# Optimization experiments

Measured on AMD Instinct MI355X. Metric: run time of the kernel, lower is better.

The kernel has to match this reference:

```python
import jax, jax.numpy as jnp
import numpy as np

B, N, K, DIM = 8, 2048, 8, 128
EPS = 1e-5  # BatchNorm eps (torch default); BN evaluated in inference mode with running stats


def _xavier(key, o, i):
    lim = float(np.sqrt(6.0 / (i + o)))
    return jax.random.uniform(key, (o, i), jnp.float32, -lim, lim)


def setup_inputs() -> dict:
    key = jax.random.key(0)
    ks = jax.random.split(key, 8)
    x = jax.random.normal(ks[0], (B, 3, N), jnp.float32)
    w0 = _xavier(ks[1], DIM, 3)
    b0 = jnp.zeros((DIM,), jnp.float32)
    ws = jnp.stack([_xavier(ks[2 + i], DIM, DIM) for i in range(2)])  # [2,DIM,DIM]
    bs = jnp.zeros((2, DIM), jnp.float32)
    # BatchNorm (eval-mode) params / running stats, mildly randomized so math is exercised
    bn_g = 1.0 + 0.1 * jax.random.normal(ks[4], (3, DIM), jnp.float32)
    bn_b = 0.1 * jax.random.normal(ks[5], (3, DIM), jnp.float32)
    bn_m = 0.1 * jax.random.normal(ks[6], (3, DIM), jnp.float32)
    bn_v = jax.random.uniform(ks[7], (3, DIM), jnp.float32, 0.5, 1.5)
    return {"x": x, "w0": w0, "b0": b0, "ws": ws, "bs": bs,
            "bn_g": bn_g, "bn_b": bn_b, "bn_m": bn_m, "bn_v": bn_v}


def _group(x):
    # x: [B,3,N] -> relative kNN coords [B,3,N,K] (torch code uses [B,3,K,N]; axis order
    # is immaterial since the MLP is pointwise and the max is over the neighbor axis)
    inner = jnp.einsum('bcn,bcm->bnm', x, x)
    sq = jnp.sum(x * x, axis=1)                      # [B,N]
    dist = sq[:, :, None] - 2.0 * inner + sq[:, None, :]
    idx = jax.lax.top_k(-dist, K)[1]                 # [B,N,K] nearest (incl. self)
    grouped = jax.vmap(lambda xi, ii: xi[:, ii])(x, idx)  # [B,3,N,K]
    return grouped - x[:, :, :, None]


def _block(h, w, b, g, be, m, v):
    # 1x1 conv + eval-mode BatchNorm + ReLU over channel axis 1
    h = jnp.einsum('oc,bcnk->bonk', w, h) + b[None, :, None, None]
    scale = (g / jnp.sqrt(v + EPS))[None, :, None, None]
    h = (h - m[None, :, None, None]) * scale + be[None, :, None, None]
    return jax.nn.relu(h)


def reference(x, w0, b0, ws, bs, bn_g, bn_b, bn_m, bn_v):
    h = _group(x)                                    # [B,3,N,K]
    h = _block(h, w0, b0, bn_g[0], bn_b[0], bn_m[0], bn_v[0])
    for i in range(2):
        h = _block(h, ws[i], bs[i], bn_g[i + 1], bn_b[i + 1], bn_m[i + 1], bn_v[i + 1])
    return jnp.max(h, axis=3)                        # [B,DIM,N]
```

## Files before the change

### kernel.cpp

```cpp
#include <hip/hip_runtime.h>


#define EPSF 1e-5f
#define FMAXV 3.402823466e+38f

#define NB 8
#define NN 2048
#define KNBR 8
#define DIMF 128
#define NQ (NB * NN)
#define NPAIR (NQ * KNBR)

#define OFF16_W1H 0
#define OFF16_W1L 16384
#define OFF16_W2H 32768
#define OFF16_W2L 49152
#define OFF_C1 32896
#define OFF_C2 33024
#define OFF_W0F 33152
#define OFF_IDX 33792

typedef __attribute__((ext_vector_type(4))) float f32x4;
typedef __attribute__((ext_vector_type(8))) short short8v;

__device__ __forceinline__ float relu_f(float a) { return fmaxf(a, 0.0f); }

__device__ __forceinline__ void split3(float f, unsigned& hi, unsigned& lo) {
  const unsigned u = __float_as_uint(f);
  const unsigned h = (u + 0x7FFFu + ((u >> 16) & 1u)) >> 16;
  const float hf = __uint_as_float(h << 16);
  lo = __float_as_uint(f - hf) >> 16;
  hi = h;
}

__device__ __forceinline__ f32x4 mfma16x16x32bf(short8v a, short8v b, f32x4 c) {
  return __builtin_amdgcn_mfma_f32_16x16x32_bf16(a, b, c, 0, 0, 0);
}

#define KCSWAP(a, b)                  \
  {                                   \
    const float mn_ = fminf(a, b);    \
    const float mx_ = fmaxf(a, b);    \
    (a) = mn_; (b) = mx_;             \
  }

#define SORT8(d0, d1, d2, d3, d4, d5, d6, d7)                   \
  KCSWAP(d0, d1) KCSWAP(d2, d3) KCSWAP(d4, d5) KCSWAP(d6, d7)   \
  KCSWAP(d0, d2) KCSWAP(d1, d3) KCSWAP(d4, d6) KCSWAP(d5, d7)   \
  KCSWAP(d1, d2) KCSWAP(d5, d6)                                 \
  KCSWAP(d0, d4) KCSWAP(d1, d5) KCSWAP(d2, d6) KCSWAP(d3, d7)   \
  KCSWAP(d2, d4) KCSWAP(d3, d5)                                 \
  KCSWAP(d1, d2) KCSWAP(d3, d4) KCSWAP(d5, d6)

#define KCLEAN8()                                               \
  KCSWAP(k0, k4) KCSWAP(k1, k5) KCSWAP(k2, k6) KCSWAP(k3, k7)   \
  KCSWAP(k0, k2) KCSWAP(k1, k3) KCSWAP(k4, k6) KCSWAP(k5, k7)   \
  KCSWAP(k0, k1) KCSWAP(k2, k3) KCSWAP(k4, k5) KCSWAP(k6, k7)

#define KFOLD8(d0, d1, d2, d3, d4, d5, d6, d7)                  \
  {                                                             \
    k0 = fminf(k0, d7); k1 = fminf(k1, d6);                     \
    k2 = fminf(k2, d5); k3 = fminf(k3, d4);                     \
    k4 = fminf(k4, d3); k5 = fminf(k5, d2);                     \
    k6 = fminf(k6, d1); k7 = fminf(k7, d0);                     \
    KCLEAN8()                                                   \
  }

#define KMERGE(mv)                                              \
  {                                                             \
    const float q0_ = __shfl_xor(k0, mv, 64);                   \
    const float q1_ = __shfl_xor(k1, mv, 64);                   \
    const float q2_ = __shfl_xor(k2, mv, 64);                   \
    const float q3_ = __shfl_xor(k3, mv, 64);                   \
    const float q4_ = __shfl_xor(k4, mv, 64);                   \
    const float q5_ = __shfl_xor(k5, mv, 64);                   \
    const float q6_ = __shfl_xor(k6, mv, 64);                   \
    const float q7_ = __shfl_xor(k7, mv, 64);                   \
    k0 = fminf(k0, q7_); k1 = fminf(k1, q6_);                   \
    k2 = fminf(k2, q5_); k3 = fminf(k3, q4_);                   \
    k4 = fminf(k4, q3_); k5 = fminf(k5, q2_);                   \
    k6 = fminf(k6, q1_); k7 = fminf(k7, q0_);                   \
    KCLEAN8()                                                   \
  }

__global__ __launch_bounds__(512, 4) void knn_kernel(
    const float* __restrict__ x, const float* __restrict__ w0,
    const float* __restrict__ b0, const float* __restrict__ wstk,
    const float* __restrict__ bstk, const float* __restrict__ g,
    const float* __restrict__ be, const float* __restrict__ bm,
    const float* __restrict__ bv, float* __restrict__ ws) {
  __shared__ float2 xyp[2080];
  __shared__ float2 zsp[2080];
  const int t = threadIdx.x;
  const int bid = blockIdx.x;

  if (bid >= 1024) {
    const int i = (bid - 1024) * 512 + t;
    unsigned short* __restrict__ wsh = (unsigned short*)ws;
    const int fo = i >> 7, k = i & 127;
    const float s1 = g[128 + fo] / sqrtf(bv[128 + fo] + EPSF);
    const float s2 = g[256 + fo] / sqrtf(bv[256 + fo] + EPSF);
    unsigned h1, l1, h2, l2;
    split3(wstk[i] * s1, h1, l1);
    split3(wstk[16384 + i] * s2, h2, l2);
    const int dst = ((fo >> 4) * 4 + (k >> 5)) * 512 +
                    (((k >> 3) & 3) * 16 + (fo & 15)) * 8 + (k & 7);
    wsh[OFF16_W1H + dst] = (unsigned short)h1;
    wsh[OFF16_W1L + dst] = (unsigned short)l1;
    wsh[OFF16_W2H + dst] = (unsigned short)h2;
    wsh[OFF16_W2L + dst] = (unsigned short)l2;
    if (bid == 1024 && t < 128) {
      const int f = t;
      const float s0 = g[f] / sqrtf(bv[f] + EPSF);
      const float s1b = g[128 + f] / sqrtf(bv[128 + f] + EPSF);
      const float s2b = g[256 + f] / sqrtf(bv[256 + f] + EPSF);
      ws[OFF_C1 + f] = (bstk[f] - bm[128 + f]) * s1b + be[128 + f];
      ws[OFF_C2 + f] = (bstk[128 + f] - bm[256 + f]) * s2b + be[256 + f];
      float4 wv;
      wv.x = w0[3 * f + 0] * s0;
      wv.y = w0[3 * f + 1] * s0;
      wv.z = w0[3 * f + 2] * s0;
      wv.w = (b0[f] - bm[f]) * s0 + be[f];
      *((float4*)(ws + OFF_W0F) + f) = wv;
    }
    return;
  }

  const int bb = bid >> 7;
  const int qloc0 = (bid & 127) * 16;
  const float* __restrict__ xb = x + bb * 3 * NN;

#pragma unroll
  for (int k = 0; k < 4; ++k) {
    const int i = t + k * 512;
    const float a0 = xb[i];
    const float a1 = xb[2048 + i];
    const float a2 = xb[4096 + i];
    const float sq = fmaf(a2, a2, fmaf(a1, a1, a0 * a0));
    const int ii = i + (i >> 6);
    xyp[ii] = make_float2(a0, a1);
    zsp[ii] = make_float2(a2, sq);
  }

  const int qi = t >> 5;
  const int sg = t & 31;
  const int n = qloc0 + qi;
  const int q = bb * NN + n;
  const float qx0 = xb[n], qx1 = xb[2048 + n], qx2 = xb[4096 + n];
  const float sqn = fmaf(qx2, qx2, fmaf(qx1, qx1, qx0 * qx0));
  __syncthreads();

  const float2* __restrict__ xr = xyp + sg * 65;
  const float2* __restrict__ zr = zsp + sg * 65;

  float dv[64];
  float k0 = FMAXV, k1 = FMAXV, k2 = FMAXV, k3 = FMAXV,
        k4 = FMAXV, k5 = FMAXV, k6 = FMAXV, k7 = FMAXV;
#pragma unroll
  for (int bt = 0; bt < 8; ++bt) {
    float d0, d1, d2, d3, d4, d5, d6, d7;
#define KD(j, dj)                                                        \
    {                                                                    \
      const float2 cxy = xr[bt * 8 + (j)];                               \
      const float2 czs = zr[bt * 8 + (j)];                               \
      const float inner =                                                \
          fmaf(qx2, czs.x, fmaf(qx1, cxy.y, qx0 * cxy.x));               \
      dj = (sqn - 2.0f * inner) + czs.y;                                 \
    }
    KD(0, d0) KD(1, d1) KD(2, d2) KD(3, d3)
    KD(4, d4) KD(5, d5) KD(6, d6) KD(7, d7)
#undef KD
    dv[bt * 8 + 0] = d0; dv[bt * 8 + 1] = d1;
    dv[bt * 8 + 2] = d2; dv[bt * 8 + 3] = d3;
    dv[bt * 8 + 4] = d4; dv[bt * 8 + 5] = d5;
    dv[bt * 8 + 6] = d6; dv[bt * 8 + 7] = d7;
    SORT8(d0, d1, d2, d3, d4, d5, d6, d7)
    KFOLD8(d0, d1, d2, d3, d4, d5, d6, d7)
  }

  KMERGE(1) KMERGE(2) KMERGE(4) KMERGE(8) KMERGE(16)
  const float thr = k7;

  unsigned am = 0, bm2 = 0;
#pragma unroll
  for (int mm = 0; mm < 32; ++mm) am |= (dv[mm] <= thr) ? (1u << mm) : 0u;
#pragma unroll
  for (int mm = 0; mm < 32; ++mm)
    bm2 |= (dv[32 + mm] <= thr) ? (1u << mm) : 0u;

  const int cnt = __popc(am) + __popc(bm2);
  int inc = cnt, tq;
  tq = __shfl_up(inc, 1, 32); inc += (sg >= 1) ? tq : 0;
  tq = __shfl_up(inc, 2, 32); inc += (sg >= 2) ? tq : 0;
  tq = __shfl_up(inc, 4, 32); inc += (sg >= 4) ? tq : 0;
  tq = __shfl_up(inc, 8, 32); inc += (sg >= 8) ? tq : 0;
  tq = __shfl_up(inc, 16, 32); inc += (sg >= 16) ? tq : 0;
  int pos = inc - cnt;

  int* __restrict__ idxg = (int*)(ws + OFF_IDX);
  {
    unsigned w = am;
    while (w) {
      const int b = __ffs(w) - 1;
      w &= w - 1;
      if (pos < 8) idxg[q * 8 + pos] = bb * NN + sg * 64 + b;
      ++pos;
    }
    w = bm2;
    while (w) {
      const int b = __ffs(w) - 1;
      w &= w - 1;
      if (pos < 8) idxg[q * 8 + pos] = bb * NN + sg * 64 + 32 + b;
      ++pos;
    }
  }
}

__global__ __launch_bounds__(256, 2) void fused_kernel(
    const float* __restrict__ x, float* __restrict__ ws,
    float* __restrict__ out) {
  extern __shared__ char smem[];
  float* __restrict__ OS = (float*)(smem + 65536);
  float4* __restrict__ W0L = (float4*)(smem + 73728);

  const int* __restrict__ idxg = (const int*)(ws + OFF_IDX);
  const unsigned short* __restrict__ wsu = (const unsigned short*)ws;

  const int t = threadIdx.x;
  const int lane = t & 63, w = t >> 6;
  const int wc = w;
  const int bid = blockIdx.x;
  const int bb = bid & 7, qseg = bid >> 3;
  const int chunk0 = bb * 512 + qseg * 8;
  const float* __restrict__ xb = x + bb * 3 * NN;

  if (t < 128) {
    const float4 wv = *((const float4*)(ws + OFF_W0F) + t);
    W0L[((t & 7) << 4) | (t >> 3)] = wv;
  }

  short8v w1h[2][4], w1l[2][4], w2h[2][4], w2l[2][4];
#pragma unroll
  for (int ft = 0; ft < 2; ++ft)
#pragma unroll
    for (int ks = 0; ks < 4; ++ks) {
      const int off = ((wc * 2 + ft) * 4 + ks) * 512 + lane * 8;
      w1h[ft][ks] = *(const short8v*)(wsu + OFF16_W1H + off);
      w1l[ft][ks] = *(const short8v*)(wsu + OFF16_W1L + off);
      w2h[ft][ks] = *(const short8v*)(wsu + OFF16_W2H + off);
      w2l[ft][ks] = *(const short8v*)(wsu + OFF16_W2L + off);
    }

  const float c1v0 = (ws + OFF_C1)[wc * 32 + (lane & 15)];
  const float c1v1 = (ws + OFF_C1)[wc * 32 + 16 + (lane & 15)];
  const float c2v0 = (ws + OFF_C2)[wc * 32 + (lane & 15)];
  const float c2v1 = (ws + OFF_C2)[wc * 32 + 16 + (lane & 15)];

  const int row = t >> 3, part8 = t & 7;
  __syncthreads();

#define PACK_WRITE_A(base, hv, kc)                              \
  {                                                             \
    unsigned hh[8], ll[8];                                      \
    _Pragma("unroll") for (int e = 0; e < 8; ++e)               \
        split3(hv[e], hh[e], ll[e]);                            \
    int4 hp, lp;                                                \
    hp.x = (int)(hh[0] | (hh[1] << 16));                        \
    hp.y = (int)(hh[2] | (hh[3] << 16));                        \
    hp.z = (int)(hh[4] | (hh[5] << 16));                        \
    hp.w = (int)(hh[6] | (hh[7] << 16));                        \
    lp.x = (int)(ll[0] | (ll[1] << 16));                        \
    lp.y = (int)(ll[2] | (ll[3] << 16));                        \
    lp.z = (int)(ll[4] | (ll[5] << 16));                        \
    lp.w = (int)(ll[6] | (ll[7] << 16));                        \
    const int col = (kc) ^ (row & 7);                           \
    *(int4*)((base) + row * 256 + col * 16) = hp;               \
    *(int4*)((base) + 8192 + row * 256 + col * 16) = lp;        \
  }

#define STAGE_A(base, R0, R1, R2)                               \
  {                                                             \
    float hv0[8], hv1[8];                                       \
    _Pragma("unroll") for (int e = 0; e < 8; ++e) {             \
      const float4 wa = W0L[e * 16 + part8 * 2];                \
      const float4 wb = W0L[e * 16 + part8 * 2 + 1];            \
      hv0[e] = relu_f(                                          \
          fmaf(wa.z, R2, fmaf(wa.y, R1, fmaf(wa.x, R0, wa.w))));\
      hv1[e] = relu_f(                                          \
          fmaf(wb.z, R2, fmaf(wb.y, R1, fmaf(wb.x, R0, wb.w))));\
    }                                                           \
    PACK_WRITE_A(base, hv0, part8 * 2)                          \
    PACK_WRITE_A(base, hv1, part8 * 2 + 1)                      \
  }

#define G1_TO_H(Abase, Hbase)                                           \
  {                                                                     \
    f32x4 acc[2][2];                                                    \
    _Pragma("unroll") for (int pt = 0; pt < 2; ++pt)                    \
        _Pragma("unroll") for (int ft = 0; ft < 2; ++ft)                \
            acc[pt][ft] = (f32x4){0.f, 0.f, 0.f, 0.f};                  \
    __builtin_amdgcn_s_setprio(1);                                      \
    _Pragma("unroll") for (int ks = 0; ks < 4; ++ks) {                  \
      const int kc = ks * 4 + (lane >> 4);                              \
      _Pragma("unroll") for (int pt = 0; pt < 2; ++pt) {                \
        const int arow = pt * 16 + (lane & 15);                         \
        const int col = kc ^ (arow & 7);                                \
        const short8v ah =                                              \
            *(const short8v*)((Abase) + arow * 256 + col * 16);         \
        const short8v al =                                              \
            *(const short8v*)((Abase) + 8192 + arow * 256 + col * 16);  \
        _Pragma("unroll") for (int ft = 0; ft < 2; ++ft) {              \
          acc[pt][ft] = mfma16x16x32bf(al, w1h[ft][ks], acc[pt][ft]);   \
          acc[pt][ft] = mfma16x16x32bf(ah, w1l[ft][ks], acc[pt][ft]);   \
          acc[pt][ft] = mfma16x16x32bf(ah, w1h[ft][ks], acc[pt][ft]);   \
        }                                                               \
      }                                                                 \
    }                                                                   \
    __builtin_amdgcn_s_setprio(0);                                      \
    unsigned* __restrict__ Hp = (unsigned*)(Hbase);                     \
    _Pragma("unroll") for (int pt = 0; pt < 2; ++pt)                    \
        _Pragma("unroll") for (int ft = 0; ft < 2; ++ft) {              \
      const int fo = wc * 32 + ft * 16 + (lane & 15);                   \
      const int cc = fo >> 2;                                           \
      const float cb = ft ? c1v1 : c1v0;                                \
      _Pragma("unroll") for (int reg = 0; reg < 4; ++reg) {             \
        const int p = pt * 16 + (lane >> 4) * 4 + reg;                  \
        const float vv = relu_f(acc[pt][ft][reg] + cb);                 \
        unsigned hh, ll;                                                \
        split3(vv, hh, ll);                                             \
        Hp[p * 128 + ((cc ^ (p & 7)) << 2) + (fo & 3)] = (hh << 16) | ll; \
      }                                                                 \
    }                                                                   \
  }

#define G2_TO_OS(Hbase, CH)                                             \
  {                                                                     \
    const unsigned* __restrict__ Hp = (const unsigned*)(Hbase);         \
    f32x4 acc2[2][2];                                                   \
    _Pragma("unroll") for (int pt = 0; pt < 2; ++pt)                    \
        _Pragma("unroll") for (int ft = 0; ft < 2; ++ft)                \
            acc2[pt][ft] = (f32x4){0.f, 0.f, 0.f, 0.f};                 \
    __builtin_amdgcn_s_setprio(1);                                      \
    _Pragma("unroll") for (int ks = 0; ks < 4; ++ks) {                  \
      const int cc0 = ks * 8 + (lane >> 4) * 2;                         \
      _Pragma("unroll") for (int pt = 0; pt < 2; ++pt) {                \
        const int p = pt * 16 + (lane & 15);                            \
        const int4 u0 = *(const int4*)&Hp[p * 128 + ((cc0 ^ (p & 7)) << 2)]; \
        const int4 u1 =                                                 \
            *(const int4*)&Hp[p * 128 + (((cc0 + 1) ^ (p & 7)) << 2)];  \
        const unsigned uu[8] = {(unsigned)u0.x, (unsigned)u0.y,         \
                                (unsigned)u0.z, (unsigned)u0.w,         \
                                (unsigned)u1.x, (unsigned)u1.y,         \
                                (unsigned)u1.z, (unsigned)u1.w};        \
        short8v ah, al;                                                 \
        _Pragma("unroll") for (int e = 0; e < 8; ++e) {                 \
          ah[e] = (short)(uu[e] >> 16);                                 \
          al[e] = (short)(uu[e] & 0xFFFFu);                             \
        }                                                               \
        _Pragma("unroll") for (int ft = 0; ft < 2; ++ft) {              \
          acc2[pt][ft] = mfma16x16x32bf(al, w2h[ft][ks], acc2[pt][ft]); \
          acc2[pt][ft] = mfma16x16x32bf(ah, w2l[ft][ks], acc2[pt][ft]); \
          acc2[pt][ft] = mfma16x16x32bf(ah, w2h[ft][ks], acc2[pt][ft]); \
        }                                                               \
      }                                                                 \
    }                                                                   \
    __builtin_amdgcn_s_setprio(0);                                      \
    const int g = lane >> 4;                                            \
    _Pragma("unroll") for (int pt = 0; pt < 2; ++pt)                    \
        _Pragma("unroll") for (int ft = 0; ft < 2; ++ft) {              \
      const int fo = wc * 32 + ft * 16 + (lane & 15);                   \
      const float cb = ft ? c2v1 : c2v0;                                \
      const float v0 = relu_f(acc2[pt][ft][0] + cb);                    \
      const float v1 = relu_f(acc2[pt][ft][1] + cb);                    \
      const float v2 = relu_f(acc2[pt][ft][2] + cb);                    \
      const float v3 = relu_f(acc2[pt][ft][3] + cb);                    \
      float m = fmaxf(fmaxf(v0, v1), fmaxf(v2, v3));                    \
      m = fmaxf(m, __shfl_xor(m, 16, 64));                              \
      if ((g & 1) == 0) {                                               \
        const int qloc = pt * 2 + (g >> 1);                             \
        OS[(((CH) & 3) * 4 + qloc) * 128 + fo] = m;                     \
      }                                                                 \
    }                                                                   \
  }

#define OS_FLUSH(h)                                                     \
  {                                                                     \
    const int f = t >> 1, sh = t & 1;                                   \
    float* __restrict__ op = out + (long)(bb * 128 + f) * 2048 +        \
                             qseg * 32 + (h) * 16 + sh * 8;             \
    float4 o1, o2;                                                      \
    o1.x = OS[(sh * 8 + 0) * 128 + f];                                  \
    o1.y = OS[(sh * 8 + 1) * 128 + f];                                  \
    o1.z = OS[(sh * 8 + 2) * 128 + f];                                  \
    o1.w = OS[(sh * 8 + 3) * 128 + f];                                  \
    o2.x = OS[(sh * 8 + 4) * 128 + f];                                  \
    o2.y = OS[(sh * 8 + 5) * 128 + f];                                  \
    o2.z = OS[(sh * 8 + 6) * 128 + f];                                  \
    o2.w = OS[(sh * 8 + 7) * 128 + f];                                  \
    *(float4*)op = o1;                                                  \
    *(float4*)(op + 4) = o2;                                            \
  }

#define LOAD_R(CH, MG, R0, R1, R2)                     \
  {                                                    \
    const int mloc = (MG) & 2047;                      \
    const int nloc = ((((CH) * 32 + row)) >> 3) & 2047;\
    R0 = xb[mloc] - xb[nloc];                          \
    R1 = xb[2048 + mloc] - xb[2048 + nloc];            \
    R2 = xb[4096 + mloc] - xb[4096 + nloc];            \
  }

  {
    const int mg0 = idxg[(chunk0 + 0) * 32 + row];
    const int mg1 = idxg[(chunk0 + 1) * 32 + row];
    float r0, r1, r2;
    LOAD_R(chunk0 + 0, mg0, r0, r1, r2)
    STAGE_A(smem, r0, r1, r2)
    __syncthreads();
    G1_TO_H(smem, smem + 32768)
    LOAD_R(chunk0 + 1, mg1, r0, r1, r2)
    STAGE_A(smem + 16384, r0, r1, r2)
    __syncthreads();
  }

#pragma unroll 1
  for (int j = 0; j < 8; ++j) {
    int mg2 = 0;
    if (j < 6) mg2 = idxg[(chunk0 + j + 2) * 32 + row];

    G2_TO_OS(smem + 32768 + (j & 1) * 16384, j)

    if (j < 7) {
      G1_TO_H(smem + ((j + 1) & 1) * 16384,
              smem + 32768 + ((j + 1) & 1) * 16384)
      if (j < 6) {
        float r0, r1, r2;
        LOAD_R(chunk0 + j + 2, mg2, r0, r1, r2)
        STAGE_A(smem + (j & 1) * 16384, r0, r1, r2)
      }
    }
    __syncthreads();
    if (j == 3) {
      OS_FLUSH(0)
      __syncthreads();
    }
  }
  OS_FLUSH(1)
}

extern "C" void kernel_launch(void* const* d_in, const int* in_sizes, int n_in,
                              void* d_out, int out_size, void* d_ws,
                              size_t ws_size, hipStream_t stream) {
  (void)in_sizes; (void)n_in; (void)out_size; (void)ws_size;
  const float* x = (const float*)d_in[0];
  const float* w0 = (const float*)d_in[1];
  const float* b0 = (const float*)d_in[2];
  const float* wst = (const float*)d_in[3];
  const float* bst = (const float*)d_in[4];
  const float* g = (const float*)d_in[5];
  const float* be = (const float*)d_in[6];
  const float* bm = (const float*)d_in[7];
  const float* bv = (const float*)d_in[8];
  float* out = (float*)d_out;
  float* ws = (float*)d_ws;

  hipFuncSetAttribute((const void*)fused_kernel,
                      hipFuncAttributeMaxDynamicSharedMemorySize, 75776);

  knn_kernel<<<1056, 512, 0, stream>>>(x, w0, b0, wst, bst, g, be, bm, bv, ws);
  fused_kernel<<<512, 256, 75776, stream>>>(x, ws, out);
}
```

Baseline: 59.28 us.

## Merge kNN search and MLP into a single kernel with per-block weight prep

Fuses the kNN search, weight/BN folding and the pointwise MLP+max into one kernel of 2048 blocks, each handling 8 queries. Neighbor indices now stay in shared memory rather than passing through a global workspace, and one kernel launch plus the global round trip are removed. In exchange, every block reloads all 16K x 2 weights from global memory and redoes the bf16 hi/lo split and BN scale math. Each block also rebuilds the full 2048-point shared table for its batch, and the MLP pipeline per block becomes very short with little overlap.

```diff
diff --git a/kernel.cpp b/kernel.cpp
--- a/kernel.cpp
+++ b/kernel.cpp
@@ -6,19 +6,6 @@
 
 #define NB 8
 #define NN 2048
-#define KNBR 8
-#define DIMF 128
-#define NQ (NB * NN)
-#define NPAIR (NQ * KNBR)
-
-#define OFF16_W1H 0
-#define OFF16_W1L 16384
-#define OFF16_W2H 32768
-#define OFF16_W2L 49152
-#define OFF_C1 32896
-#define OFF_C2 33024
-#define OFF_W0F 33152
-#define OFF_IDX 33792
 
 typedef __attribute__((ext_vector_type(4))) float f32x4;
 typedef __attribute__((ext_vector_type(8))) short short8v;
@@ -83,56 +70,39 @@
     KCLEAN8()                                                   \
   }
 
-__global__ __launch_bounds__(512, 4) void knn_kernel(
+__global__ __launch_bounds__(256, 2) void mega_kernel(
     const float* __restrict__ x, const float* __restrict__ w0,
     const float* __restrict__ b0, const float* __restrict__ wstk,
     const float* __restrict__ bstk, const float* __restrict__ g,
     const float* __restrict__ be, const float* __restrict__ bm,
-    const float* __restrict__ bv, float* __restrict__ ws) {
-  __shared__ float2 xyp[2080];
-  __shared__ float2 zsp[2080];
+    const float* __restrict__ bv, float* __restrict__ out) {
+  extern __shared__ char smem[];
+  float2* __restrict__ xyp = (float2*)smem;
+  float2* __restrict__ zsp = (float2*)(smem + 16640);
+  float* __restrict__ OS = (float*)(smem + 65536);
+  float4* __restrict__ W0L = (float4*)(smem + 69632);
+  int* __restrict__ idxs = (int*)(smem + 71680);
+
   const int t = threadIdx.x;
+  const int lane = t & 63, w = t >> 6;
+  const int wc = w;
   const int bid = blockIdx.x;
-
-  if (bid >= 1024) {
-    const int i = (bid - 1024) * 512 + t;
-    unsigned short* __restrict__ wsh = (unsigned short*)ws;
-    const int fo = i >> 7, k = i & 127;
-    const float s1 = g[128 + fo] / sqrtf(bv[128 + fo] + EPSF);
-    const float s2 = g[256 + fo] / sqrtf(bv[256 + fo] + EPSF);
-    unsigned h1, l1, h2, l2;
-    split3(wstk[i] * s1, h1, l1);
-    split3(wstk[16384 + i] * s2, h2, l2);
-    const int dst = ((fo >> 4) * 4 + (k >> 5)) * 512 +
-                    (((k >> 3) & 3) * 16 + (fo & 15)) * 8 + (k & 7);
-    wsh[OFF16_W1H + dst] = (unsigned short)h1;
-    wsh[OFF16_W1L + dst] = (unsigned short)l1;
-    wsh[OFF16_W2H + dst] = (unsigned short)h2;
-    wsh[OFF16_W2L + dst] = (unsigned short)l2;
-    if (bid == 1024 && t < 128) {
-      const int f = t;
-      const float s0 = g[f] / sqrtf(bv[f] + EPSF);
-      const float s1b = g[128 + f] / sqrtf(bv[128 + f] + EPSF);
-      const float s2b = g[256 + f] / sqrtf(bv[256 + f] + EPSF);
-      ws[OFF_C1 + f] = (bstk[f] - bm[128 + f]) * s1b + be[128 + f];
-      ws[OFF_C2 + f] = (bstk[128 + f] - bm[256 + f]) * s2b + be[256 + f];
-      float4 wv;
-      wv.x = w0[3 * f + 0] * s0;
-      wv.y = w0[3 * f + 1] * s0;
-      wv.z = w0[3 * f + 2] * s0;
-      wv.w = (b0[f] - bm[f]) * s0 + be[f];
-      *((float4*)(ws + OFF_W0F) + f) = wv;
-    }
-    return;
-  }
-
-  const int bb = bid >> 7;
-  const int qloc0 = (bid & 127) * 16;
+  const int bb = bid & 7, qseg = bid >> 3;
   const float* __restrict__ xb = x + bb * 3 * NN;
 
-#pragma unroll
-  for (int k = 0; k < 4; ++k) {
-    const int i = t + k * 512;
+  if (t < 128) {
+    const float s0 = g[t] / sqrtf(bv[t] + EPSF);
+    float4 wv;
+    wv.x = w0[3 * t + 0] * s0;
+    wv.y = w0[3 * t + 1] * s0;
+    wv.z = w0[3 * t + 2] * s0;
+    wv.w = (b0[t] - bm[t]) * s0 + be[t];
+    W0L[((t & 7) << 4) | (t >> 3)] = wv;
+  }
+
+#pragma unroll
+  for (int k = 0; k < 8; ++k) {
+    const int i = t + k * 256;
     const float a0 = xb[i];
     const float a1 = xb[2048 + i];
     const float a2 = xb[4096 + i];
@@ -144,120 +114,120 @@
 
   const int qi = t >> 5;
   const int sg = t & 31;
-  const int n = qloc0 + qi;
-  const int q = bb * NN + n;
+  const int n = qseg * 8 + qi;
   const float qx0 = xb[n], qx1 = xb[2048 + n], qx2 = xb[4096 + n];
   const float sqn = fmaf(qx2, qx2, fmaf(qx1, qx1, qx0 * qx0));
   __syncthreads();
 
-  const float2* __restrict__ xr = xyp + sg * 65;
-  const float2* __restrict__ zr = zsp + sg * 65;
-
-  float dv[64];
-  float k0 = FMAXV, k1 = FMAXV, k2 = FMAXV, k3 = FMAXV,
-        k4 = FMAXV, k5 = FMAXV, k6 = FMAXV, k7 = FMAXV;
-#pragma unroll
-  for (int bt = 0; bt < 8; ++bt) {
-    float d0, d1, d2, d3, d4, d5, d6, d7;
+  {
+    const float2* __restrict__ xr = xyp + sg * 65;
+    const float2* __restrict__ zr = zsp + sg * 65;
+
+    float dv[64];
+    float k0 = FMAXV, k1 = FMAXV, k2 = FMAXV, k3 = FMAXV,
+          k4 = FMAXV, k5 = FMAXV, k6 = FMAXV, k7 = FMAXV;
+#pragma unroll
+    for (int bt = 0; bt < 8; ++bt) {
+      float d0, d1, d2, d3, d4, d5, d6, d7;
 #define KD(j, dj)                                                        \
-    {                                                                    \
-      const float2 cxy = xr[bt * 8 + (j)];                               \
-      const float2 czs = zr[bt * 8 + (j)];                               \
-      const float inner =                                                \
-          fmaf(qx2, czs.x, fmaf(qx1, cxy.y, qx0 * cxy.x));               \
-      dj = (sqn - 2.0f * inner) + czs.y;                                 \
+      {                                                                  \
+        const float2 cxy = xr[bt * 8 + (j)];                             \
+        const float2 czs = zr[bt * 8 + (j)];                             \
+        const float inner =                                              \
+            fmaf(qx2, czs.x, fmaf(qx1, cxy.y, qx0 * cxy.x));             \
+        dj = (sqn - 2.0f * inner) + czs.y;                               \
+      }
+      KD(0, d0) KD(1, d1) KD(2, d2) KD(3, d3)
+      KD(4, d4) KD(5, d5) KD(6, d6) KD(7, d7)
+#undef KD
+      dv[bt * 8 + 0] = d0; dv[bt * 8 + 1] = d1;
+      dv[bt * 8 + 2] = d2; dv[bt * 8 + 3] = d3;
+      dv[bt * 8 + 4] = d4; dv[bt * 8 + 5] = d5;
+      dv[bt * 8 + 6] = d6; dv[bt * 8 + 7] = d7;
+      SORT8(d0, d1, d2, d3, d4, d5, d6, d7)
+      KFOLD8(d0, d1, d2, d3, d4, d5, d6, d7)
     }
-    KD(0, d0) KD(1, d1) KD(2, d2) KD(3, d3)
-    KD(4, d4) KD(5, d5) KD(6, d6) KD(7, d7)
-#undef KD
-    dv[bt * 8 + 0] = d0; dv[bt * 8 + 1] = d1;
-    dv[bt * 8 + 2] = d2; dv[bt * 8 + 3] = d3;
-    dv[bt * 8 + 4] = d4; dv[bt * 8 + 5] = d5;
-    dv[bt * 8 + 6] = d6; dv[bt * 8 + 7] = d7;
-    SORT8(d0, d1, d2, d3, d4, d5, d6, d7)
-    KFOLD8(d0, d1, d2, d3, d4, d5, d6, d7)
-  }
-
-  KMERGE(1) KMERGE(2) KMERGE(4) KMERGE(8) KMERGE(16)
-  const float thr = k7;
-
-  unsigned am = 0, bm2 = 0;
-#pragma unroll
-  for (int mm = 0; mm < 32; ++mm) am |= (dv[mm] <= thr) ? (1u << mm) : 0u;
-#pragma unroll
-  for (int mm = 0; mm < 32; ++mm)
-    bm2 |= (dv[32 + mm] <= thr) ? (1u << mm) : 0u;
-
-  const int cnt = __popc(am) + __popc(bm2);
-  int inc = cnt, tq;
-  tq = __shfl_up(inc, 1, 32); inc += (sg >= 1) ? tq : 0;
-  tq = __shfl_up(inc, 2, 32); inc += (sg >= 2) ? tq : 0;
-  tq = __shfl_up(inc, 4, 32); inc += (sg >= 4) ? tq : 0;
-  tq = __shfl_up(inc, 8, 32); inc += (sg >= 8) ? tq : 0;
-  tq = __shfl_up(inc, 16, 32); inc += (sg >= 16) ? tq : 0;
-  int pos = inc - cnt;
-
-  int* __restrict__ idxg = (int*)(ws + OFF_IDX);
+
+    KMERGE(1) KMERGE(2) KMERGE(4) KMERGE(8) KMERGE(16)
+    const float thr = k7;
+
+    unsigned am = 0, bm2 = 0;
+#pragma unroll
+    for (int mm = 0; mm < 32; ++mm) am |= (dv[mm] <= thr) ? (1u << mm) : 0u;
+#pragma unroll
+    for (int mm = 0; mm < 32; ++mm)
+      bm2 |= (dv[32 + mm] <= thr) ? (1u << mm) : 0u;
+
+    const int cnt = __popc(am) + __popc(bm2);
+    int inc = cnt, tq;
+    tq = __shfl_up(inc, 1, 32); inc += (sg >= 1) ? tq : 0;
+    tq = __shfl_up(inc, 2, 32); inc += (sg >= 2) ? tq : 0;
+    tq = __shfl_up(inc, 4, 32); inc += (sg >= 4) ? tq : 0;
+    tq = __shfl_up(inc, 8, 32); inc += (sg >= 8) ? tq : 0;
+    tq = __shfl_up(inc, 16, 32); inc += (sg >= 16) ? tq : 0;
+    int pos = inc - cnt;
+
+    {
+      unsigned wv = am;
+      while (wv) {
+        const int b = __ffs(wv) - 1;
+        wv &= wv - 1;
+        if (pos < 8) idxs[qi * 8 + pos] = sg * 64 + b;
+        ++pos;
+      }
+      wv = bm2;
+      while (wv) {
+        const int b = __ffs(wv) - 1;
+        wv &= wv - 1;
+        if (pos < 8) idxs[qi * 8 + pos] = sg * 64 + 32 + b;
+        ++pos;
+      }
+    }
+  }
+  __syncthreads();
+
+  short8v w1h[2][4], w1l[2][4], w2h[2][4], w2l[2][4];
+#pragma unroll
+  for (int ft = 0; ft < 2; ++ft) {
+    const int fo = wc * 32 + ft * 16 + (lane & 15);
+    const float s1 = g[128 + fo] / sqrtf(bv[128 + fo] + EPSF);
+    const float s2 = g[256 + fo] / sqrtf(bv[256 + fo] + EPSF);
+#pragma unroll
+    for (int ks = 0; ks < 4; ++ks) {
+      const int kb = ks * 32 + (lane >> 4) * 8;
+      const float4 a1 = *(const float4*)(wstk + fo * 128 + kb);
+      const float4 b1 = *(const float4*)(wstk + fo * 128 + kb + 4);
+      const float4 a2 = *(const float4*)(wstk + 16384 + fo * 128 + kb);
+      const float4 b2 = *(const float4*)(wstk + 16384 + fo * 128 + kb + 4);
+      const float v1[8] = {a1.x, a1.y, a1.z, a1.w, b1.x, b1.y, b1.z, b1.w};
+      const float v2[8] = {a2.x, a2.y, a2.z, a2.w, b2.x, b2.y, b2.z, b2.w};
+      short8v h1v, l1v, h2v, l2v;
+#pragma unroll
+      for (int e = 0; e < 8; ++e) {
+        unsigned hh, ll;
+        split3(v1[e] * s1, hh, ll);
+        h1v[e] = (short)hh; l1v[e] = (short)ll;
+        split3(v2[e] * s2, hh, ll);
+        h2v[e] = (short)hh; l2v[e] = (short)ll;
+      }
+      w1h[ft][ks] = h1v; w1l[ft][ks] = l1v;
+      w2h[ft][ks] = h2v; w2l[ft][ks] = l2v;
+    }
+  }
+  float c1v0, c1v1, c2v0, c2v1;
   {
-    unsigned w = am;
-    while (w) {
-      const int b = __ffs(w) - 1;
-      w &= w - 1;
-      if (pos < 8) idxg[q * 8 + pos] = bb * NN + sg * 64 + b;
-      ++pos;
-    }
-    w = bm2;
-    while (w) {
-      const int b = __ffs(w) - 1;
-      w &= w - 1;
-      if (pos < 8) idxg[q * 8 + pos] = bb * NN + sg * 64 + 32 + b;
-      ++pos;
-    }
-  }
-}
-
-__global__ __launch_bounds__(256, 2) void fused_kernel(
-    const float* __restrict__ x, float* __restrict__ ws,
-    float* __restrict__ out) {
-  extern __shared__ char smem[];
-  float* __restrict__ OS = (float*)(smem + 65536);
-  float4* __restrict__ W0L = (float4*)(smem + 73728);
-
-  const int* __restrict__ idxg = (const int*)(ws + OFF_IDX);
-  const unsigned short* __restrict__ wsu = (const unsigned short*)ws;
-
-  const int t = threadIdx.x;
-  const int lane = t & 63, w = t >> 6;
-  const int wc = w;
-  const int bid = blockIdx.x;
-  const int bb = bid & 7, qseg = bid >> 3;
-  const int chunk0 = bb * 512 + qseg * 8;
-  const float* __restrict__ xb = x + bb * 3 * NN;
-
-  if (t < 128) {
-    const float4 wv = *((const float4*)(ws + OFF_W0F) + t);
-    W0L[((t & 7) << 4) | (t >> 3)] = wv;
-  }
-
-  short8v w1h[2][4], w1l[2][4], w2h[2][4], w2l[2][4];
-#pragma unroll
-  for (int ft = 0; ft < 2; ++ft)
-#pragma unroll
-    for (int ks = 0; ks < 4; ++ks) {
-      const int off = ((wc * 2 + ft) * 4 + ks) * 512 + lane * 8;
-      w1h[ft][ks] = *(const short8v*)(wsu + OFF16_W1H + off);
-      w1l[ft][ks] = *(const short8v*)(wsu + OFF16_W1L + off);
-      w2h[ft][ks] = *(const short8v*)(wsu + OFF16_W2H + off);
-      w2l[ft][ks] = *(const short8v*)(wsu + OFF16_W2L + off);
-    }
-
-  const float c1v0 = (ws + OFF_C1)[wc * 32 + (lane & 15)];
-  const float c1v1 = (ws + OFF_C1)[wc * 32 + 16 + (lane & 15)];
-  const float c2v0 = (ws + OFF_C2)[wc * 32 + (lane & 15)];
-  const float c2v1 = (ws + OFF_C2)[wc * 32 + 16 + (lane & 15)];
+    const int foA = wc * 32 + (lane & 15), foB = foA + 16;
+    const float s1A = g[128 + foA] / sqrtf(bv[128 + foA] + EPSF);
+    const float s1B = g[128 + foB] / sqrtf(bv[128 + foB] + EPSF);
+    const float s2A = g[256 + foA] / sqrtf(bv[256 + foA] + EPSF);
+    const float s2B = g[256 + foB] / sqrtf(bv[256 + foB] + EPSF);
+    c1v0 = (bstk[foA] - bm[128 + foA]) * s1A + be[128 + foA];
+    c1v1 = (bstk[foB] - bm[128 + foB]) * s1B + be[128 + foB];
+    c2v0 = (bstk[128 + foA] - bm[256 + foA]) * s2A + be[256 + foA];
+    c2v1 = (bstk[128 + foB] - bm[256 + foB]) * s2B + be[256 + foB];
+  }
 
   const int row = t >> 3, part8 = t & 7;
-  __syncthreads();
 
 #define PACK_WRITE_A(base, hv, kc)                              \
   {                                                             \
@@ -365,7 +335,7 @@
       }                                                                 \
     }                                                                   \
     __builtin_amdgcn_s_setprio(0);                                      \
-    const int g = lane >> 4;                                            \
+    const int gg = lane >> 4;                                           \
     _Pragma("unroll") for (int pt = 0; pt < 2; ++pt)                    \
         _Pragma("unroll") for (int ft = 0; ft < 2; ++ft) {              \
       const int fo = wc * 32 + ft * 16 + (lane & 15);                   \
@@ -376,82 +346,59 @@
       const float v3 = relu_f(acc2[pt][ft][3] + cb);                    \
       float m = fmaxf(fmaxf(v0, v1), fmaxf(v2, v3));                    \
       m = fmaxf(m, __shfl_xor(m, 16, 64));                              \
-      if ((g & 1) == 0) {                                               \
-        const int qloc = pt * 2 + (g >> 1);                             \
-        OS[(((CH) & 3) * 4 + qloc) * 128 + fo] = m;                     \
+      if ((gg & 1) == 0) {                                              \
+        const int qloc = pt * 2 + (gg >> 1);                            \
+        OS[((CH) * 4 + qloc) * 128 + fo] = m;                          \
       }                                                                 \
     }                                                                   \
   }
 
-#define OS_FLUSH(h)                                                     \
-  {                                                                     \
-    const int f = t >> 1, sh = t & 1;                                   \
-    float* __restrict__ op = out + (long)(bb * 128 + f) * 2048 +        \
-                             qseg * 32 + (h) * 16 + sh * 8;             \
-    float4 o1, o2;                                                      \
-    o1.x = OS[(sh * 8 + 0) * 128 + f];                                  \
-    o1.y = OS[(sh * 8 + 1) * 128 + f];                                  \
-    o1.z = OS[(sh * 8 + 2) * 128 + f];                                  \
-    o1.w = OS[(sh * 8 + 3) * 128 + f];                                  \
-    o2.x = OS[(sh * 8 + 4) * 128 + f];                                  \
-    o2.y = OS[(sh * 8 + 5) * 128 + f];                                  \
-    o2.z = OS[(sh * 8 + 6) * 128 + f];                                  \
-    o2.w = OS[(sh * 8 + 7) * 128 + f];                                  \
-    *(float4*)op = o1;                                                  \
-    *(float4*)(op + 4) = o2;                                            \
-  }
-
-#define LOAD_R(CH, MG, R0, R1, R2)                     \
-  {                                                    \
-    const int mloc = (MG) & 2047;                      \
-    const int nloc = ((((CH) * 32 + row)) >> 3) & 2047;\
-    R0 = xb[mloc] - xb[nloc];                          \
-    R1 = xb[2048 + mloc] - xb[2048 + nloc];            \
-    R2 = xb[4096 + mloc] - xb[4096 + nloc];            \
+#define LOAD_R(C, R0, R1, R2)                                  \
+  {                                                            \
+    const int pl = (qseg * 2 + (C)) * 32 + row;                \
+    const int nloc = pl >> 3;                                  \
+    const int mloc = idxs[(nloc - qseg * 8) * 8 + (pl & 7)];   \
+    R0 = xb[mloc] - xb[nloc];                                  \
+    R1 = xb[2048 + mloc] - xb[2048 + nloc];                    \
+    R2 = xb[4096 + mloc] - xb[4096 + nloc];                    \
   }
 
   {
-    const int mg0 = idxg[(chunk0 + 0) * 32 + row];
-    const int mg1 = idxg[(chunk0 + 1) * 32 + row];
     float r0, r1, r2;
-    LOAD_R(chunk0 + 0, mg0, r0, r1, r2)
+    LOAD_R(0, r0, r1, r2)
     STAGE_A(smem, r0, r1, r2)
-    __syncthreads();
-    G1_TO_H(smem, smem + 32768)
-    LOAD_R(chunk0 + 1, mg1, r0, r1, r2)
+  }
+  __syncthreads();
+  G1_TO_H(smem, smem + 32768)
+  {
+    float r0, r1, r2;
+    LOAD_R(1, r0, r1, r2)
     STAGE_A(smem + 16384, r0, r1, r2)
-    __syncthreads();
-  }
-
-#pragma unroll 1
-  for (int j = 0; j < 8; ++j) {
-    int mg2 = 0;
-    if (j < 6) mg2 = idxg[(chunk0 + j + 2) * 32 + row];
-
-    G2_TO_OS(smem + 32768 + (j & 1) * 16384, j)
-
-    if (j < 7) {
-      G1_TO_H(smem + ((j + 1) & 1) * 16384,
-              smem + 32768 + ((j + 1) & 1) * 16384)
-      if (j < 6) {
-        float r0, r1, r2;
-        LOAD_R(chunk0 + j + 2, mg2, r0, r1, r2)
-        STAGE_A(smem + (j & 1) * 16384, r0, r1, r2)
-      }
-    }
-    __syncthreads();
-    if (j == 3) {
-      OS_FLUSH(0)
-      __syncthreads();
-    }
-  }
-  OS_FLUSH(1)
+  }
+  __syncthreads();
+  G2_TO_OS(smem + 32768, 0)
+  G1_TO_H(smem + 16384, smem + 49152)
+  __syncthreads();
+  G2_TO_OS(smem + 49152, 1)
+  __syncthreads();
+
+  {
+    const int f = t >> 1, sh = t & 1;
+    float* __restrict__ op =
+        out + (long)(bb * 128 + f) * 2048 + qseg * 8 + sh * 4;
+    float4 o;
+    o.x = OS[(sh * 4 + 0) * 128 + f];
+    o.y = OS[(sh * 4 + 1) * 128 + f];
+    o.z = OS[(sh * 4 + 2) * 128 + f];
+    o.w = OS[(sh * 4 + 3) * 128 + f];
+    *(float4*)op = o;
+  }
 }
 
 extern "C" void kernel_launch(void* const* d_in, const int* in_sizes, int n_in,
                               void* d_out, int out_size, void* d_ws,
                               size_t ws_size, hipStream_t stream) {
-  (void)in_sizes; (void)n_in; (void)out_size; (void)ws_size;
+  (void)in_sizes; (void)n_in; (void)out_size; (void)d_ws; (void)ws_size;
   const float* x = (const float*)d_in[0];
   const float* w0 = (const float*)d_in[1];
   const float* b0 = (const float*)d_in[2];
@@ -462,11 +409,10 @@
   const float* bm = (const float*)d_in[7];
   const float* bv = (const float*)d_in[8];
   float* out = (float*)d_out;
-  float* ws = (float*)d_ws;
-
-  hipFuncSetAttribute((const void*)fused_kernel,
-                      hipFuncAttributeMaxDynamicSharedMemorySize, 75776);
-
-  knn_kernel<<<1056, 512, 0, stream>>>(x, w0, b0, wst, bst, g, be, bm, bv, ws);
-  fused_kernel<<<512, 256, 75776, stream>>>(x, ws, out);
+
+  hipFuncSetAttribute((const void*)mega_kernel,
+                      hipFuncAttributeMaxDynamicSharedMemorySize, 71936);
+
+  mega_kernel<<<2048, 256, 71936, stream>>>(x, w0, b0, wst, bst, g, be, bm,
+                                            bv, out);
 }
```

Result: slower. 107.7 us (+81.7%).
